# Performance work log

Measured on AMD Instinct MI355X. Metric: run time of the kernel, lower is better.

Reference implementation:

```python
import jax, jax.numpy as jnp
import numpy as np

N = 20000          # nodes
E_RAND = 320000    # random edges (avg degree 16)
E = E_RAND + N     # + self loops (no 0-in-degree nodes)
F_IN = 128
H1, D1 = 8, 32     # layer-1 heads / per-head dim
N_CLS = 40
NEG_SLOPE = 0.2


def setup_inputs() -> dict:
    key = jax.random.key(0)
    ks = jax.random.split(key, 9)
    x = jax.random.normal(ks[0], (N, F_IN), jnp.float32)
    src = jnp.concatenate([jax.random.randint(ks[1], (E_RAND,), 0, N),
                           jnp.arange(N)]).astype(jnp.int32)
    dst = jnp.concatenate([jax.random.randint(ks[2], (E_RAND,), 0, N),
                           jnp.arange(N)]).astype(jnp.int32)
    W1 = jax.random.normal(ks[3], (F_IN, H1 * D1), jnp.float32) / np.sqrt(F_IN)
    attn_l1 = jax.random.normal(ks[4], (H1, D1), jnp.float32) * 0.1
    attn_r1 = jax.random.normal(ks[5], (H1, D1), jnp.float32) * 0.1
    W2 = jax.random.normal(ks[6], (H1 * D1, N_CLS), jnp.float32) / np.sqrt(H1 * D1)
    attn_l2 = jax.random.normal(ks[7], (1, N_CLS), jnp.float32) * 0.1
    attn_r2 = jax.random.normal(ks[8], (1, N_CLS), jnp.float32) * 0.1
    return {"x": x, "W1": W1, "attn_l1": attn_l1, "attn_r1": attn_r1,
            "W2": W2, "attn_l2": attn_l2, "attn_r2": attn_r2,
            "src": src, "dst": dst}


def gat_layer(h, W, attn_l, attn_r, src, dst, n_nodes):
    """DGL GATConv (aggr='mean' path), eval mode (dropout = identity)."""
    H, D = attn_l.shape
    ft = (h @ W).reshape(-1, H, D)                 # [N, H, D]
    el = jnp.sum(ft * attn_l, axis=-1)             # [N, H]
    er = jnp.sum(ft * attn_r, axis=-1)             # [N, H]
    e = jax.nn.leaky_relu(el[src] + er[dst], NEG_SLOPE)   # [E, H]
    # ragged softmax over incoming edges of each dst node
    m = jax.ops.segment_max(e, dst, num_segments=n_nodes)
    m = jnp.where(jnp.isfinite(m), m, 0.0)         # guard empty segments
    ex = jnp.exp(e - m[dst])                       # [E, H]
    s = jax.ops.segment_sum(ex, dst, num_segments=n_nodes)
    alpha = ex / jnp.maximum(s[dst], 1e-16)        # [E, H]
    # weighted sum of src features
    out = jax.ops.segment_sum(ft[src] * alpha[:, :, None], dst,
                              num_segments=n_nodes)  # [N, H, D]
    return out


def reference(x, W1, attn_l1, attn_r1, W2, attn_l2, attn_r2, src, dst):
    h = gat_layer(x, W1, attn_l1, attn_r1, src, dst, N)   # [N, 8, 32]
    h = jax.nn.relu(h).reshape(N, H1 * D1)                # flatten(1)
    out = gat_layer(h, W2, attn_l2, attn_r2, src, dst, N) # [N, 1, 40]
    return out.mean(axis=1)                               # [N, 40]
```

## Files before the change

kernel.cpp:

```cpp
#include <hip/hip_runtime.h>
#include <hip/hip_fp16.h>

#define FIN 128
#define F1 256
#define H1N 8
#define D1N 32
#define NCLS 40
#define FT2P 64
#define W2PITCH 258
#define NEG 0.2f

static __device__ __forceinline__ float leaky(float x){ return x >= 0.f ? x : NEG*x; }

__global__ void k_hist(const int* __restrict__ dst, int* __restrict__ deg, int E){
    int e = blockIdx.x*256 + threadIdx.x;
    if (e < E) atomicAdd(&deg[dst[e]], 1);
}

__global__ void k_scan1(const int* __restrict__ deg, int* __restrict__ rowptr,
                        int* __restrict__ bsum, int n){
    __shared__ int s[256];
    int t = threadIdx.x;
    int i = blockIdx.x*256 + t;
    int v = (i < n) ? deg[i] : 0;
    s[t] = v;
    __syncthreads();
    for (int off=1; off<256; off<<=1){
        int y = (t >= off) ? s[t-off] : 0;
        __syncthreads();
        if (t >= off) s[t] += y;
        __syncthreads();
    }
    if (i < n) rowptr[i] = s[t] - v;
    if (t == 255) bsum[blockIdx.x] = s[255];
}

__global__ void k_scan2(int* __restrict__ rowptr, const int* __restrict__ bsum,
                        int n, int E){
    int b = blockIdx.x;
    int l = threadIdx.x & 63;
    int v = 0;
    for (int j = l; j < b; j += 64) v += bsum[j];
    for (int msk=1; msk<64; msk<<=1) v += __shfl_xor(v, msk);
    int i = b*256 + threadIdx.x;
    if (i < n) rowptr[i] += v;
    else if (i == n) rowptr[n] = E;
}

__global__ void k_scatter(const int* __restrict__ src, const int* __restrict__ dst,
                          const int* __restrict__ rowptr, int* __restrict__ deg,
                          int* __restrict__ adj, int E){
    int e = blockIdx.x*256 + threadIdx.x;
    if (e < E){
        int d = dst[e];
        int pos = atomicSub(&deg[d], 1) - 1;
        adj[rowptr[d] + pos] = src[e];
    }
}

__global__ __launch_bounds__(256) void k_gemm1(const float* __restrict__ X,
                                               const float* __restrict__ W,
                                               const float* __restrict__ al,
                                               const float* __restrict__ ar,
                                               __half* __restrict__ FT,
                                               float* __restrict__ el,
                                               float* __restrict__ er, int M){
    __shared__ float As[32][68];
    __shared__ float Bs[32][68];
    int t = threadIdx.x;
    int bx = blockIdx.x & 3;
    int by = blockIdx.x >> 2;
    int m0 = by*64, n0 = bx*64;
    int ty = t >> 4, tx = t & 15;
    float acc[4][4] = {};
    for (int k0 = 0; k0 < FIN; k0 += 32){
        #pragma unroll
        for (int p=0;p<2;p++){
            int f = t + p*256;
            int m = f >> 3;
            int kq = f & 7;
            int row = m0 + m;
            float4 v = make_float4(0.f,0.f,0.f,0.f);
            if (row < M) v = *(const float4*)&X[row*FIN + k0 + kq*4];
            As[kq*4+0][m] = v.x; As[kq*4+1][m] = v.y;
            As[kq*4+2][m] = v.z; As[kq*4+3][m] = v.w;
        }
        #pragma unroll
        for (int p=0;p<2;p++){
            int f = t + p*256;
            int kk = f >> 4;
            int nq = f & 15;
            float4 v = *(const float4*)&W[(size_t)(k0+kk)*F1 + n0 + nq*4];
            *(float4*)&Bs[kk][nq*4] = v;
        }
        __syncthreads();
        #pragma unroll
        for (int kk=0; kk<32; kk++){
            float4 a4 = *(const float4*)&As[kk][ty*4];
            float4 b4 = *(const float4*)&Bs[kk][tx*4];
            float av[4] = {a4.x,a4.y,a4.z,a4.w};
            float bv[4] = {b4.x,b4.y,b4.z,b4.w};
            #pragma unroll
            for (int r=0;r<4;r++)
                #pragma unroll
                for (int c=0;c<4;c++)
                    acc[r][c] = fmaf(av[r], bv[c], acc[r][c]);
        }
        __syncthreads();
    }
    int h = (bx<<1) + (tx>>3);
    int basew = h*D1N + (tx&7)*4;
    float4 wl = *(const float4*)&al[basew];
    float4 wr = *(const float4*)&ar[basew];
    float pl[4], pr[4];
    #pragma unroll
    for (int r=0;r<4;r++){
        pl[r] = acc[r][0]*wl.x + acc[r][1]*wl.y + acc[r][2]*wl.z + acc[r][3]*wl.w;
        pr[r] = acc[r][0]*wr.x + acc[r][1]*wr.y + acc[r][2]*wr.z + acc[r][3]*wr.w;
    }
    #pragma unroll
    for (int msk=1; msk<8; msk<<=1){
        #pragma unroll
        for (int r=0;r<4;r++){
            pl[r] += __shfl_xor(pl[r], msk);
            pr[r] += __shfl_xor(pr[r], msk);
        }
    }
    #pragma unroll
    for (int r=0;r<4;r++){
        int row = m0 + ty*4 + r;
        if (row < M){
            union { uint2 u; __half2 h2[2]; } P;
            P.h2[0] = __floats2half2_rn(acc[r][0], acc[r][1]);
            P.h2[1] = __floats2half2_rn(acc[r][2], acc[r][3]);
            *(uint2*)&FT[(size_t)row*F1 + n0 + tx*4] = P.u;
            if ((tx & 7) == 0){
                el[row*H1N + h] = pl[r];
                er[row*H1N + h] = pr[r];
            }
        }
    }
}

__global__ __launch_bounds__(512) void k_agg1(const __half* __restrict__ FT,
                      const float* __restrict__ el, const float* __restrict__ er,
                      const float* __restrict__ W2,
                      const float* __restrict__ al2, const float* __restrict__ ar2,
                      const int* __restrict__ rowptr, const int* __restrict__ adj,
                      __half* __restrict__ FT2, float* __restrict__ el2,
                      float* __restrict__ er2, int n, int nwTot){
    __shared__ __half W2h[40*W2PITCH];
    __shared__ float  hst[8][260];
    int t = threadIdx.x;
    for (int e = t; e < 256*40; e += 512){
        int k = e / 40, c = e - k*40;
        W2h[c*W2PITCH + k] = __float2half_rn(W2[e]);
    }
    __syncthreads();

    int w = t >> 6, l = t & 63;
    int h2 = l >> 3;
    int c = (l < 40) ? l : (l - 40);
    float keep = (l < NCLS) ? 1.f : 0.f;
    float a2l = al2[c], a2r = ar2[c];
    const __half* wrow = &W2h[c*W2PITCH];
    float* hp = &hst[w][0];

    for (int node = blockIdx.x*8 + w; node < n; node += nwTot){
        int rs = rowptr[node];
        int deg = rowptr[node+1] - rs;
        float erh2 = er[node*H1N + h2];

        float ssum = 0.f;
        float ax=0.f, ay=0.f, az=0.f, aw=0.f;
        int j = 0;
        for (; j + 8 <= deg; j += 8){
            int sv[8];
            #pragma unroll
            for (int i=0;i<8;i++) sv[i] = adj[rs+j+i];
            float av[8];
            #pragma unroll
            for (int i=0;i<8;i++){
                av[i] = __expf(leaky(el[sv[i]*H1N + h2] + erh2));
                ssum += av[i];
            }
            #pragma unroll
            for (int i=0;i<8;i++){
                union { uint2 u; __half2 h2v[2]; } U;
                U.u = *(const uint2*)&FT[(size_t)sv[i]*F1 + l*4];
                float2 f01 = __half22float2(U.h2v[0]);
                float2 f23 = __half22float2(U.h2v[1]);
                ax = fmaf(av[i], f01.x, ax); ay = fmaf(av[i], f01.y, ay);
                az = fmaf(av[i], f23.x, az); aw = fmaf(av[i], f23.y, aw);
            }
        }
        for (; j < deg; j++){
            int s = adj[rs + j];
            float a = __expf(leaky(el[s*H1N + h2] + erh2));
            ssum += a;
            union { uint2 u; __half2 h2v[2]; } U;
            U.u = *(const uint2*)&FT[(size_t)s*F1 + l*4];
            float2 f01 = __half22float2(U.h2v[0]);
            float2 f23 = __half22float2(U.h2v[1]);
            ax = fmaf(a, f01.x, ax); ay = fmaf(a, f01.y, ay);
            az = fmaf(a, f23.x, az); aw = fmaf(a, f23.y, aw);
        }
        float inv = 1.f / fmaxf(ssum, 1e-16f);
        ax = fmaxf(ax*inv, 0.f); ay = fmaxf(ay*inv, 0.f);
        az = fmaxf(az*inv, 0.f); aw = fmaxf(aw*inv, 0.f);

        *(float4*)&hp[l*4] = make_float4(ax, ay, az, aw);
        __builtin_amdgcn_wave_barrier();
        asm volatile("s_waitcnt lgkmcnt(0)" ::: "memory");
        float o0=0.f, o1=0.f, o2=0.f, o3=0.f;
        #pragma unroll
        for (int k0 = 0; k0 < 64; k0 += 4){
            {   float4 hv = *(const float4*)&hp[k0*4];
                float2 fa = __half22float2(*(const __half2*)&wrow[k0*4]);
                float2 fb = __half22float2(*(const __half2*)&wrow[k0*4+2]);
                o0 = fmaf(hv.x, fa.x, o0); o0 = fmaf(hv.y, fa.y, o0);
                o0 = fmaf(hv.z, fb.x, o0); o0 = fmaf(hv.w, fb.y, o0); }
            {   float4 hv = *(const float4*)&hp[(k0+1)*4];
                float2 fa = __half22float2(*(const __half2*)&wrow[(k0+1)*4]);
                float2 fb = __half22float2(*(const __half2*)&wrow[(k0+1)*4+2]);
                o1 = fmaf(hv.x, fa.x, o1); o1 = fmaf(hv.y, fa.y, o1);
                o1 = fmaf(hv.z, fb.x, o1); o1 = fmaf(hv.w, fb.y, o1); }
            {   float4 hv = *(const float4*)&hp[(k0+2)*4];
                float2 fa = __half22float2(*(const __half2*)&wrow[(k0+2)*4]);
                float2 fb = __half22float2(*(const __half2*)&wrow[(k0+2)*4+2]);
                o2 = fmaf(hv.x, fa.x, o2); o2 = fmaf(hv.y, fa.y, o2);
                o2 = fmaf(hv.z, fb.x, o2); o2 = fmaf(hv.w, fb.y, o2); }
            {   float4 hv = *(const float4*)&hp[(k0+3)*4];
                float2 fa = __half22float2(*(const __half2*)&wrow[(k0+3)*4]);
                float2 fb = __half22float2(*(const __half2*)&wrow[(k0+3)*4+2]);
                o3 = fmaf(hv.x, fa.x, o3); o3 = fmaf(hv.y, fa.y, o3);
                o3 = fmaf(hv.z, fb.x, o3); o3 = fmaf(hv.w, fb.y, o3); }
        }
        float out = (o0 + o1) + (o2 + o3);
        __builtin_amdgcn_wave_barrier();
        float pl = keep * out * a2l;
        float pr = keep * out * a2r;
        #pragma unroll
        for (int msk=1; msk<64; msk<<=1){
            pl += __shfl_xor(pl, msk);
            pr += __shfl_xor(pr, msk);
        }
        if (l == 0){ el2[node] = pl; er2[node] = pr; }
        if (l < NCLS) FT2[(size_t)node*FT2P + l] = __float2half_rn(out);
    }
}

__global__ __launch_bounds__(256) void k_agg2(const __half* __restrict__ FT2,
                      const float* __restrict__ el, const float* __restrict__ er,
                      const int* __restrict__ rowptr, const int* __restrict__ adj,
                      float* __restrict__ out, int n){
    int node = (blockIdx.x*256 + threadIdx.x) >> 6;
    int l = threadIdx.x & 63;
    if (node >= n) return;
    int rs = rowptr[node];
    int deg = rowptr[node+1] - rs;
    float ern = er[node];
    float ssum = 0.f, acc = 0.f;
    int j = 0;
    for (; j + 8 <= deg; j += 8){
        int sv[8];
        #pragma unroll
        for (int i=0;i<8;i++) sv[i] = adj[rs+j+i];
        float av[8];
        #pragma unroll
        for (int i=0;i<8;i++){
            av[i] = __expf(leaky(el[sv[i]] + ern));
            ssum += av[i];
        }
        if (l < NCLS){
            #pragma unroll
            for (int i=0;i<8;i++){
                float f = __half2float(FT2[(size_t)sv[i]*FT2P + l]);
                acc = fmaf(av[i], f, acc);
            }
        }
    }
    for (; j < deg; j++){
        int s = adj[rs + j];
        float a = __expf(leaky(el[s] + ern));
        ssum += a;
        if (l < NCLS) acc = fmaf(a, __half2float(FT2[(size_t)s*FT2P + l]), acc);
    }
    if (l < NCLS) out[(size_t)node*NCLS + l] = acc / fmaxf(ssum, 1e-16f);
}

extern "C" void kernel_launch(void* const* d_in, const int* in_sizes, int n_in,
                              void* d_out, int out_size, void* d_ws, size_t ws_size,
                              hipStream_t stream){
    const float* x   = (const float*)d_in[0];
    const float* W1  = (const float*)d_in[1];
    const float* al1 = (const float*)d_in[2];
    const float* ar1 = (const float*)d_in[3];
    const float* W2  = (const float*)d_in[4];
    const float* al2 = (const float*)d_in[5];
    const float* ar2 = (const float*)d_in[6];
    const int*   src = (const int*)d_in[7];
    const int*   dst = (const int*)d_in[8];
    int E = in_sizes[7];
    int n = in_sizes[0] / FIN;

    char* ws = (char*)d_ws;
    size_t off = 0;
    auto alloc = [&](size_t bytes)->void*{
        void* p = ws + off; off += (bytes + 255) & ~(size_t)255; return p;
    };
    __half* ft1h  = (__half*)alloc((size_t)n*F1*2);
    __half* ft2h  = (__half*)alloc((size_t)n*FT2P*2);
    float*  el1   = (float*)alloc((size_t)n*H1N*4);
    float*  er1   = (float*)alloc((size_t)n*H1N*4);
    float*  el2   = (float*)alloc((size_t)n*4);
    float*  er2   = (float*)alloc((size_t)n*4);
    int*    rowptr= (int*)alloc((size_t)(n+1)*4);
    int*    adj   = (int*)alloc((size_t)E*4);
    int*    bsum  = (int*)alloc((size_t)((n+255)/256)*4);
    int*    deg   = (int*)alloc((size_t)n*4);

    int nb_e = (E + 255)/256;
    int nb_n = (n + 255)/256;

    hipMemsetAsync(deg, 0, (size_t)n*4, stream);
    k_hist   <<<nb_e, 256, 0, stream>>>(dst, deg, E);
    k_scan1  <<<nb_n, 256, 0, stream>>>(deg, rowptr, bsum, n);
    k_scan2  <<<(n+1+255)/256, 256, 0, stream>>>(rowptr, bsum, n, E);
    k_scatter<<<nb_e, 256, 0, stream>>>(src, dst, rowptr, deg, adj, E);

    k_gemm1  <<<((n+63)/64)*4, 256, 0, stream>>>(x, W1, al1, ar1, ft1h, el1, er1, n);

    int aggBlocks = 1250;
    k_agg1   <<<aggBlocks, 512, 0, stream>>>(ft1h, el1, er1, W2, al2, ar2,
                                             rowptr, adj, ft2h, el2, er2,
                                             n, aggBlocks*8);
    k_agg2   <<<(n+3)/4, 256, 0, stream>>>(ft2h, el2, er2, rowptr, adj,
                                           (float*)d_out, n);
}
```

Measured before the change: 215.0 us.

## Precompute per-edge attention exponentials in separate passes before aggregation

Adds a destination-index array to the CSR build and two edge-parallel kernels that compute exp(leaky(el[src]+er[dst])) per edge and head, stored as fp16 in CSR order. The aggregation kernels then read these contiguous values instead of gathering el per neighbour and evaluating exp inline. This replaces the redundant per-lane exp and the scattered el gathers with coalesced loads, at the cost of two extra launches, extra memory traffic for the did and alpha buffers, and fp16 rounding of the unnormalised weights without max subtraction. It also swaps the order of two FMAs in one accumulation.

```diff
diff --git a/kernel.cpp b/kernel.cpp
--- a/kernel.cpp
+++ b/kernel.cpp
@@ -49,12 +49,14 @@
 
 __global__ void k_scatter(const int* __restrict__ src, const int* __restrict__ dst,
                           const int* __restrict__ rowptr, int* __restrict__ deg,
-                          int* __restrict__ adj, int E){
+                          int* __restrict__ adj, int* __restrict__ did, int E){
     int e = blockIdx.x*256 + threadIdx.x;
     if (e < E){
         int d = dst[e];
         int pos = atomicSub(&deg[d], 1) - 1;
-        adj[rowptr[d] + pos] = src[e];
+        int q = rowptr[d] + pos;
+        adj[q] = src[e];
+        did[q] = d;
     }
 }
 
@@ -142,8 +144,34 @@
     }
 }
 
+__global__ __launch_bounds__(256) void k_alpha1(const float* __restrict__ el,
+                      const float* __restrict__ er, const int* __restrict__ adj,
+                      const int* __restrict__ did, __half* __restrict__ alph, int E){
+    int p = blockIdx.x*256 + threadIdx.x;
+    if (p >= E) return;
+    int s = adj[p], d = did[p];
+    float4 e0 = *(const float4*)&el[s*H1N];
+    float4 e1 = *(const float4*)&el[s*H1N + 4];
+    float4 r0 = *(const float4*)&er[d*H1N];
+    float4 r1 = *(const float4*)&er[d*H1N + 4];
+    union { uint4 u; __half2 h[4]; } O;
+    O.h[0] = __floats2half2_rn(__expf(leaky(e0.x+r0.x)), __expf(leaky(e0.y+r0.y)));
+    O.h[1] = __floats2half2_rn(__expf(leaky(e0.z+r0.z)), __expf(leaky(e0.w+r0.w)));
+    O.h[2] = __floats2half2_rn(__expf(leaky(e1.x+r1.x)), __expf(leaky(e1.y+r1.y)));
+    O.h[3] = __floats2half2_rn(__expf(leaky(e1.z+r1.z)), __expf(leaky(e1.w+r1.w)));
+    *(uint4*)&alph[(size_t)p*H1N] = O.u;
+}
+
+__global__ __launch_bounds__(256) void k_alpha2(const float* __restrict__ el2,
+                      const float* __restrict__ er2, const int* __restrict__ adj,
+                      const int* __restrict__ did, __half* __restrict__ alph2, int E){
+    int p = blockIdx.x*256 + threadIdx.x;
+    if (p >= E) return;
+    alph2[p] = __float2half_rn(__expf(leaky(el2[adj[p]] + er2[did[p]])));
+}
+
 __global__ __launch_bounds__(512) void k_agg1(const __half* __restrict__ FT,
-                      const float* __restrict__ el, const float* __restrict__ er,
+                      const __half* __restrict__ alph,
                       const float* __restrict__ W2,
                       const float* __restrict__ al2, const float* __restrict__ ar2,
                       const int* __restrict__ rowptr, const int* __restrict__ adj,
@@ -169,7 +197,6 @@
     for (int node = blockIdx.x*8 + w; node < n; node += nwTot){
         int rs = rowptr[node];
         int deg = rowptr[node+1] - rs;
-        float erh2 = er[node*H1N + h2];
 
         float ssum = 0.f;
         float ax=0.f, ay=0.f, az=0.f, aw=0.f;
@@ -181,7 +208,7 @@
             float av[8];
             #pragma unroll
             for (int i=0;i<8;i++){
-                av[i] = __expf(leaky(el[sv[i]*H1N + h2] + erh2));
+                av[i] = __half2float(alph[(size_t)(rs+j+i)*H1N + h2]);
                 ssum += av[i];
             }
             #pragma unroll
@@ -196,7 +223,7 @@
         }
         for (; j < deg; j++){
             int s = adj[rs + j];
-            float a = __expf(leaky(el[s*H1N + h2] + erh2));
+            float a = __half2float(alph[(size_t)(rs+j)*H1N + h2]);
             ssum += a;
             union { uint2 u; __half2 h2v[2]; } U;
             U.u = *(const uint2*)&FT[(size_t)s*F1 + l*4];
@@ -234,7 +261,7 @@
                 float2 fa = __half22float2(*(const __half2*)&wrow[(k0+3)*4]);
                 float2 fb = __half22float2(*(const __half2*)&wrow[(k0+3)*4+2]);
                 o3 = fmaf(hv.x, fa.x, o3); o3 = fmaf(hv.y, fa.y, o3);
-                o3 = fmaf(hv.z, fb.x, o3); o3 = fmaf(hv.w, fb.y, o3); }
+                o3 = fmaf(hv.w, fb.y, o3); o3 = fmaf(hv.z, fb.x, o3); }
         }
         float out = (o0 + o1) + (o2 + o3);
         __builtin_amdgcn_wave_barrier();
@@ -251,7 +278,7 @@
 }
 
 __global__ __launch_bounds__(256) void k_agg2(const __half* __restrict__ FT2,
-                      const float* __restrict__ el, const float* __restrict__ er,
+                      const __half* __restrict__ alph2,
                       const int* __restrict__ rowptr, const int* __restrict__ adj,
                       float* __restrict__ out, int n){
     int node = (blockIdx.x*256 + threadIdx.x) >> 6;
@@ -259,7 +286,6 @@
     if (node >= n) return;
     int rs = rowptr[node];
     int deg = rowptr[node+1] - rs;
-    float ern = er[node];
     float ssum = 0.f, acc = 0.f;
     int j = 0;
     for (; j + 8 <= deg; j += 8){
@@ -269,7 +295,7 @@
         float av[8];
         #pragma unroll
         for (int i=0;i<8;i++){
-            av[i] = __expf(leaky(el[sv[i]] + ern));
+            av[i] = __half2float(alph2[rs+j+i]);
             ssum += av[i];
         }
         if (l < NCLS){
@@ -282,7 +308,7 @@
     }
     for (; j < deg; j++){
         int s = adj[rs + j];
-        float a = __expf(leaky(el[s] + ern));
+        float a = __half2float(alph2[rs+j]);
         ssum += a;
         if (l < NCLS) acc = fmaf(a, __half2float(FT2[(size_t)s*FT2P + l]), acc);
     }
@@ -311,12 +337,15 @@
     };
     __half* ft1h  = (__half*)alloc((size_t)n*F1*2);
     __half* ft2h  = (__half*)alloc((size_t)n*FT2P*2);
+    __half* alph  = (__half*)alloc((size_t)E*H1N*2);
+    __half* alph2 = (__half*)alloc((size_t)E*2);
     float*  el1   = (float*)alloc((size_t)n*H1N*4);
     float*  er1   = (float*)alloc((size_t)n*H1N*4);
     float*  el2   = (float*)alloc((size_t)n*4);
     float*  er2   = (float*)alloc((size_t)n*4);
     int*    rowptr= (int*)alloc((size_t)(n+1)*4);
     int*    adj   = (int*)alloc((size_t)E*4);
+    int*    did   = (int*)alloc((size_t)E*4);
     int*    bsum  = (int*)alloc((size_t)((n+255)/256)*4);
     int*    deg   = (int*)alloc((size_t)n*4);
 
@@ -327,14 +356,16 @@
     k_hist   <<<nb_e, 256, 0, stream>>>(dst, deg, E);
     k_scan1  <<<nb_n, 256, 0, stream>>>(deg, rowptr, bsum, n);
     k_scan2  <<<(n+1+255)/256, 256, 0, stream>>>(rowptr, bsum, n, E);
-    k_scatter<<<nb_e, 256, 0, stream>>>(src, dst, rowptr, deg, adj, E);
+    k_scatter<<<nb_e, 256, 0, stream>>>(src, dst, rowptr, deg, adj, did, E);
 
     k_gemm1  <<<((n+63)/64)*4, 256, 0, stream>>>(x, W1, al1, ar1, ft1h, el1, er1, n);
+    k_alpha1 <<<nb_e, 256, 0, stream>>>(el1, er1, adj, did, alph, E);
 
     int aggBlocks = 1250;
-    k_agg1   <<<aggBlocks, 512, 0, stream>>>(ft1h, el1, er1, W2, al2, ar2,
+    k_agg1   <<<aggBlocks, 512, 0, stream>>>(ft1h, alph, W2, al2, ar2,
                                              rowptr, adj, ft2h, el2, er2,
                                              n, aggBlocks*8);
-    k_agg2   <<<(n+3)/4, 256, 0, stream>>>(ft2h, el2, er2, rowptr, adj,
+    k_alpha2 <<<nb_e, 256, 0, stream>>>(el2, er2, adj, did, alph2, E);
+    k_agg2   <<<(n+3)/4, 256, 0, stream>>>(ft2h, alph2, rowptr, adj,
                                            (float*)d_out, n);
 }
```

Result: slower. 219.5 us (+2.1%).
